# Performance work log

Hardware: AMD Instinct MI355X
Metric: run time of the kernel (lower is better)

The kernel has to match this reference:

```python
import jax, jax.numpy as jnp
import numpy as np

MARGIN = 1.0


def setup_inputs() -> dict:
    key = jax.random.key(0)
    k1, k2 = jax.random.split(key)
    embeddings = jax.random.normal(k1, (4096, 512), dtype=jnp.float32)
    labels = jax.random.randint(k2, (4096,), 0, 256, dtype=jnp.int32)
    return {"embeddings": embeddings, "labels": labels}


def _masked_random_gather(dist, mask, key):
    # Uniformly sample one valid (masked-True) column per row via argmax of
    # uniform noise restricted to the mask (equivalent to torch.randint over
    # the per-row index list, fully vectorized). Rows with no valid entry -> 0.
    B = dist.shape[0]
    u = jax.random.uniform(key, mask.shape)          # [B, B] in [0, 1)
    idx = jnp.argmax(jnp.where(mask, u, -1.0), axis=1)  # [B]
    has_valid = jnp.any(mask, axis=1)
    d = dist[jnp.arange(B), idx]
    return jnp.where(has_valid, d, 0.0)


def reference(embeddings, labels):
    B = embeddings.shape[0]
    # Pairwise squared Euclidean distances: ||a||^2 + ||b||^2 - 2 a.b, clamped >= 0
    dot = embeddings @ embeddings.T                  # [B, B]
    sq = jnp.diagonal(dot)                           # [B]
    dist = jax.nn.relu(sq[None, :] + sq[:, None] - 2.0 * dot)

    same = labels[:, None] == labels[None, :]        # [B, B]
    eye = jnp.eye(B, dtype=bool)
    mask_pos = same & ~eye
    mask_neg = ~same

    kp, kn = jax.random.split(jax.random.key(42))
    positive_dist = _masked_random_gather(dist, mask_pos, kp)
    negative_dist = _masked_random_gather(dist, mask_neg, kn)

    triplet_loss = jax.nn.relu(positive_dist - negative_dist + MARGIN)
    valid = jnp.sum(triplet_loss > 1e-16)
    return jnp.where(valid == 0, jnp.float32(0.0), jnp.mean(triplet_loss))
```

## Files before the change

### kernel.cpp

```cpp
#include <hip/hip_runtime.h>
#include <stdint.h>

#define B 4096
#define D 512

#define NB_NEG 2048

__host__ __device__ __forceinline__ uint32_t rotl32(uint32_t x, int d) {
#ifdef __HIP_DEVICE_COMPILE__
    return __builtin_amdgcn_alignbit(x, x, (uint32_t)(32 - d));
#else
    return (x << d) | (x >> (32 - d));
#endif
}

__host__ __device__ __forceinline__ void tf2x32(uint32_t k0, uint32_t k1,
                                                uint32_t x0, uint32_t x1,
                                                uint32_t& o0, uint32_t& o1) {
    const uint32_t k2 = k0 ^ k1 ^ 0x1BD11BDAu;
#define TF_ROUND(r) { x0 += x1; x1 = rotl32(x1, r); x1 ^= x0; }
    x0 += k0; x1 += k1;
    TF_ROUND(13) TF_ROUND(15) TF_ROUND(26) TF_ROUND(6)
    x0 += k1; x1 += k2 + 1u;
    TF_ROUND(17) TF_ROUND(29) TF_ROUND(16) TF_ROUND(24)
    x0 += k2; x1 += k0 + 2u;
    TF_ROUND(13) TF_ROUND(15) TF_ROUND(26) TF_ROUND(6)
    x0 += k0; x1 += k1 + 3u;
    TF_ROUND(17) TF_ROUND(29) TF_ROUND(16) TF_ROUND(24)
    x0 += k1; x1 += k2 + 4u;
    TF_ROUND(13) TF_ROUND(15) TF_ROUND(26) TF_ROUND(6)
    x0 += k2; x1 += k0 + 5u;
#undef TF_ROUND
    o0 = x0; o1 = x1;
}

__device__ __forceinline__ uint32_t draw32(uint32_t k0, uint32_t k1,
                                           uint32_t flat) {
    uint32_t o0, o1;
    tf2x32(k0, k1, 0u, flat, o0, o1);
    return o0 ^ o1;
}

__device__ __forceinline__ unsigned long long umax64(unsigned long long a,
                                                     unsigned long long b) {
    return a > b ? a : b;
}

__device__ __forceinline__ unsigned long long packbest(int bestv, int bestc) {
    return (bestv < 0)
               ? 0ull
               : ((((unsigned long long)(uint32_t)bestv + 1ull) << 12) |
                  (unsigned long long)(uint32_t)(4095 - bestc));
}

__global__ __launch_bounds__(256) void neg_bucket_kernel(
        const int* __restrict__ labels, int* __restrict__ idxn,
        int* __restrict__ bstart, unsigned short* __restrict__ bcols,
        uint32_t kn0, uint32_t kn1) {
    __shared__ int cnt[256];
    __shared__ int basex[256];
    __shared__ int fillc[256];
    __shared__ unsigned long long red[2][4];

    const int bid = blockIdx.x;
    const int t = threadIdx.x;
    const int lane = t & 63;
    const int w = t >> 6;

    if (bid == 0) {
        const int4* lp = (const int4*)(labels + (t << 4));
        const int4 La = lp[0], Lb = lp[1], Lc = lp[2], Ld = lp[3];
        const int lab16[16] = {La.x, La.y, La.z, La.w, Lb.x, Lb.y, Lb.z, Lb.w,
                               Lc.x, Lc.y, Lc.z, Lc.w, Ld.x, Ld.y, Ld.z, Ld.w};
        cnt[t] = 0;
        fillc[t] = 0;
        __syncthreads();
#pragma unroll
        for (int j = 0; j < 16; ++j) atomicAdd(&cnt[lab16[j]], 1);
        __syncthreads();
        basex[t] = cnt[t];
        __syncthreads();
        for (int off = 1; off < 256; off <<= 1) {
            const int u = (t >= off) ? basex[t - off] : 0;
            __syncthreads();
            basex[t] += u;
            __syncthreads();
        }
        bstart[t] = basex[t] - cnt[t];
        if (t == 255) bstart[256] = B;
#pragma unroll
        for (int j = 0; j < 16; ++j) {
            const int l = lab16[j];
            const int off = atomicAdd(&fillc[l], 1);
            bcols[basex[l] - cnt[l] + off] = (unsigned short)((t << 4) + j);
        }
        __syncthreads();
    }

    const int r0 = bid * 2;
    const int4* lp = (const int4*)(labels + (t << 4));
    const int4 La = lp[0], Lb = lp[1], Lc = lp[2], Ld = lp[3];
    const int lab16[16] = {La.x, La.y, La.z, La.w, Lb.x, Lb.y, Lb.z, Lb.w,
                           Lc.x, Lc.y, Lc.z, Lc.w, Ld.x, Ld.y, Ld.z, Ld.w};
    const int labr0 = labels[r0];
    const int labr1 = labels[r0 + 1];
    const uint32_t f0 = ((uint32_t)r0 << 12) + ((uint32_t)t << 4);
    int bv0 = -1, bc0 = 0, bv1 = -1, bc1 = 0;
#pragma unroll
    for (int j = 0; j < 16; ++j) {
        const int c = (t << 4) + j;
        const uint32_t h0 = draw32(kn0, kn1, f0 + (uint32_t)j);
        const uint32_t h1 = draw32(kn0, kn1, f0 + (uint32_t)j + 4096u);
        const int v0 = (int)(h0 >> 9);
        const int v1 = (int)(h1 >> 9);
        if ((lab16[j] != labr0) & (v0 > bv0)) { bv0 = v0; bc0 = c; }
        if ((lab16[j] != labr1) & (v1 > bv1)) { bv1 = v1; bc1 = c; }
    }
    unsigned long long p0 = packbest(bv0, bc0);
    unsigned long long p1 = packbest(bv1, bc1);
#pragma unroll
    for (int off = 32; off > 0; off >>= 1) {
        p0 = umax64(p0, __shfl_down(p0, off));
        p1 = umax64(p1, __shfl_down(p1, off));
    }
    if (lane == 0) { red[0][w] = p0; red[1][w] = p1; }
    __syncthreads();
    if (t < 2) {
        unsigned long long best = red[t][0];
#pragma unroll
        for (int k = 1; k < 4; ++k) best = umax64(best, red[t][k]);
        idxn[r0 + t] = best ? (int)(4095u - (uint32_t)(best & 0xFFFull)) : -1;
    }
}

__global__ __launch_bounds__(256) void loss_kernel(
        const float* __restrict__ E, const int* __restrict__ labels,
        const int* __restrict__ bstart, const unsigned short* __restrict__ bcols,
        const int* __restrict__ idxn, float* __restrict__ tl,
        uint32_t kp0, uint32_t kp1) {
    const int lane = threadIdx.x & 63;
    const int w = threadIdx.x >> 6;
    const int r = blockIdx.x * 4 + w;

    const int l = labels[r];
    const int s0 = bstart[l];
    const int s1 = bstart[l + 1];
    const uint32_t rbase = (uint32_t)r << 12;
    unsigned long long best = 0ull;
    for (int i = s0 + lane; i < s1; i += 64) {
        const int c = (int)bcols[i];
        if (c == r) continue;
        const uint32_t bits = draw32(kp0, kp1, rbase + (uint32_t)c);
        const unsigned long long pack =
            ((((unsigned long long)(bits >> 9)) + 1ull) << 12) |
            (unsigned long long)(uint32_t)(4095 - c);
        best = umax64(best, pack);
    }
#pragma unroll
    for (int off = 32; off > 0; off >>= 1)
        best = umax64(best, __shfl_xor(best, off));
    const int ip = best ? (int)(4095u - (uint32_t)(best & 0xFFFull)) : -1;
    const int in_ = idxn[r];

    const float4* er = (const float4*)(E + (size_t)r * D);
    float4 a0 = er[lane * 2];
    float4 a1 = er[lane * 2 + 1];
    float aa = a0.x * a0.x + a0.y * a0.y + a0.z * a0.z + a0.w * a0.w +
               a1.x * a1.x + a1.y * a1.y + a1.z * a1.z + a1.w * a1.w;
    float dp = 0.f, pp = 0.f, dn = 0.f, nn = 0.f;
    if (ip >= 0) {
        const float4* ep = (const float4*)(E + (size_t)ip * D);
        float4 b0 = ep[lane * 2];
        float4 b1 = ep[lane * 2 + 1];
        dp = a0.x * b0.x + a0.y * b0.y + a0.z * b0.z + a0.w * b0.w +
             a1.x * b1.x + a1.y * b1.y + a1.z * b1.z + a1.w * b1.w;
        pp = b0.x * b0.x + b0.y * b0.y + b0.z * b0.z + b0.w * b0.w +
             b1.x * b1.x + b1.y * b1.y + b1.z * b1.z + b1.w * b1.w;
    }
    if (in_ >= 0) {
        const float4* en = (const float4*)(E + (size_t)in_ * D);
        float4 c0 = en[lane * 2];
        float4 c1 = en[lane * 2 + 1];
        dn = a0.x * c0.x + a0.y * c0.y + a0.z * c0.z + a0.w * c0.w +
             a1.x * c1.x + a1.y * c1.y + a1.z * c1.z + a1.w * c1.w;
        nn = c0.x * c0.x + c0.y * c0.y + c0.z * c0.z + c0.w * c0.w +
             c1.x * c1.x + c1.y * c1.y + c1.z * c1.z + c1.w * c1.w;
    }
#pragma unroll
    for (int off = 32; off > 0; off >>= 1) {
        aa += __shfl_down(aa, off);
        dp += __shfl_down(dp, off);
        pp += __shfl_down(pp, off);
        dn += __shfl_down(dn, off);
        nn += __shfl_down(nn, off);
    }
    if (lane == 0) {
        const float pd = (ip >= 0) ? fmaxf(aa + pp - 2.0f * dp, 0.f) : 0.f;
        const float nd = (in_ >= 0) ? fmaxf(aa + nn - 2.0f * dn, 0.f) : 0.f;
        tl[r] = fmaxf(pd - nd + 1.0f, 0.f);
    }
}

__global__ __launch_bounds__(256) void finalize_kernel(
        const float* __restrict__ tl, float* __restrict__ out) {
    const int t = threadIdx.x;
    float s = 0.f;
    int c = 0;
    for (int j = t; j < B; j += 256) {
        const float v = tl[j];
        s += v;
        if (v > 1e-16f) c++;
    }
#pragma unroll
    for (int off = 32; off > 0; off >>= 1) {
        s += __shfl_down(s, off);
        c += __shfl_down(c, off);
    }
    __shared__ float ss[4];
    __shared__ int sc[4];
    if ((t & 63) == 0) { ss[t >> 6] = s; sc[t >> 6] = c; }
    __syncthreads();
    if (t == 0) {
#pragma unroll
        for (int k = 1; k < 4; ++k) { s += ss[k]; c += sc[k]; }
        out[0] = (c == 0) ? 0.0f : s * (1.0f / 4096.0f);
    }
}

extern "C" void kernel_launch(void* const* d_in, const int* in_sizes, int n_in,
                              void* d_out, int out_size, void* d_ws,
                              size_t ws_size, hipStream_t stream) {
    const float* E = (const float*)d_in[0];
    const int* labels = (const int*)d_in[1];
    float* out = (float*)d_out;

    char* ws = (char*)d_ws;
    int* idxn = (int*)(ws);
    float* tl = (float*)(ws + 16384);
    int* bstart = (int*)(ws + 32768);
    unsigned short* bcols = (unsigned short*)(ws + 36864);

    uint32_t kp0, kp1, kn0, kn1;
    tf2x32(0u, 42u, 0u, 0u, kp0, kp1);
    tf2x32(0u, 42u, 0u, 1u, kn0, kn1);

    neg_bucket_kernel<<<NB_NEG, 256, 0, stream>>>(labels, idxn, bstart, bcols,
                                                  kn0, kn1);
    loss_kernel<<<B / 4, 256, 0, stream>>>(E, labels, bstart, bcols, idxn, tl,
                                           kp0, kp1);
    finalize_kernel<<<1, 256, 0, stream>>>(tl, out);
}
```

Measured before the change: 47.23 us.

## Fuse negative sampling, positive sampling and loss into one kernel

Merges the negative-sampling kernel and the loss kernel into one kernel that handles two rows per block. The per-label bucket build is dropped; positive sampling now scans the labels each thread already holds and draws random numbers only for same-label columns. Only warps 0-1 of each block then compute the distances. This removes a kernel launch, the bucket-building serial block and the global idx round trip, but leaves two of four warps idle in the distance phase and adds a divergent per-column branch in the positive loop.

```diff
diff --git a/kernel.cpp b/kernel.cpp
--- a/kernel.cpp
+++ b/kernel.cpp
@@ -53,49 +53,18 @@
                   (unsigned long long)(uint32_t)(4095 - bestc));
 }
 
-__global__ __launch_bounds__(256) void neg_bucket_kernel(
-        const int* __restrict__ labels, int* __restrict__ idxn,
-        int* __restrict__ bstart, unsigned short* __restrict__ bcols,
-        uint32_t kn0, uint32_t kn1) {
-    __shared__ int cnt[256];
-    __shared__ int basex[256];
-    __shared__ int fillc[256];
-    __shared__ unsigned long long red[2][4];
+__global__ __launch_bounds__(256) void fused_kernel(
+        const float* __restrict__ E, const int* __restrict__ labels,
+        float* __restrict__ tl, uint32_t kp0, uint32_t kp1, uint32_t kn0,
+        uint32_t kn1) {
+    __shared__ unsigned long long redn[2][4];
+    __shared__ unsigned long long redp[2][4];
+    __shared__ int sidx[4];
 
     const int bid = blockIdx.x;
     const int t = threadIdx.x;
     const int lane = t & 63;
     const int w = t >> 6;
-
-    if (bid == 0) {
-        const int4* lp = (const int4*)(labels + (t << 4));
-        const int4 La = lp[0], Lb = lp[1], Lc = lp[2], Ld = lp[3];
-        const int lab16[16] = {La.x, La.y, La.z, La.w, Lb.x, Lb.y, Lb.z, Lb.w,
-                               Lc.x, Lc.y, Lc.z, Lc.w, Ld.x, Ld.y, Ld.z, Ld.w};
-        cnt[t] = 0;
-        fillc[t] = 0;
-        __syncthreads();
-#pragma unroll
-        for (int j = 0; j < 16; ++j) atomicAdd(&cnt[lab16[j]], 1);
-        __syncthreads();
-        basex[t] = cnt[t];
-        __syncthreads();
-        for (int off = 1; off < 256; off <<= 1) {
-            const int u = (t >= off) ? basex[t - off] : 0;
-            __syncthreads();
-            basex[t] += u;
-            __syncthreads();
-        }
-        bstart[t] = basex[t] - cnt[t];
-        if (t == 255) bstart[256] = B;
-#pragma unroll
-        for (int j = 0; j < 16; ++j) {
-            const int l = lab16[j];
-            const int off = atomicAdd(&fillc[l], 1);
-            bcols[basex[l] - cnt[l] + off] = (unsigned short)((t << 4) + j);
-        }
-        __syncthreads();
-    }
 
     const int r0 = bid * 2;
     const int4* lp = (const int4*)(labels + (t << 4));
@@ -105,6 +74,7 @@
     const int labr0 = labels[r0];
     const int labr1 = labels[r0 + 1];
     const uint32_t f0 = ((uint32_t)r0 << 12) + ((uint32_t)t << 4);
+
     int bv0 = -1, bc0 = 0, bv1 = -1, bc1 = 0;
 #pragma unroll
     for (int j = 0; j < 16; ++j) {
@@ -116,88 +86,95 @@
         if ((lab16[j] != labr0) & (v0 > bv0)) { bv0 = v0; bc0 = c; }
         if ((lab16[j] != labr1) & (v1 > bv1)) { bv1 = v1; bc1 = c; }
     }
-    unsigned long long p0 = packbest(bv0, bc0);
-    unsigned long long p1 = packbest(bv1, bc1);
+
+    int pv0 = -1, pc0 = 0, pv1 = -1, pc1 = 0;
+#pragma unroll 1
+    for (int j = 0; j < 16; ++j) {
+        const int c = (t << 4) + j;
+        const bool m0 = (lab16[j] == labr0) && (c != r0);
+        const bool m1 = (lab16[j] == labr1) && (c != r0 + 1);
+        if (m0) {
+            const uint32_t h = draw32(kp0, kp1, f0 + (uint32_t)j);
+            const int v = (int)(h >> 9);
+            if (v > pv0) { pv0 = v; pc0 = c; }
+        }
+        if (m1) {
+            const uint32_t h = draw32(kp0, kp1, f0 + (uint32_t)j + 4096u);
+            const int v = (int)(h >> 9);
+            if (v > pv1) { pv1 = v; pc1 = c; }
+        }
+    }
+
+    unsigned long long n0 = packbest(bv0, bc0);
+    unsigned long long n1 = packbest(bv1, bc1);
+    unsigned long long q0 = packbest(pv0, pc0);
+    unsigned long long q1 = packbest(pv1, pc1);
 #pragma unroll
     for (int off = 32; off > 0; off >>= 1) {
-        p0 = umax64(p0, __shfl_down(p0, off));
-        p1 = umax64(p1, __shfl_down(p1, off));
-    }
-    if (lane == 0) { red[0][w] = p0; red[1][w] = p1; }
+        n0 = umax64(n0, __shfl_down(n0, off));
+        n1 = umax64(n1, __shfl_down(n1, off));
+        q0 = umax64(q0, __shfl_down(q0, off));
+        q1 = umax64(q1, __shfl_down(q1, off));
+    }
+    if (lane == 0) {
+        redn[0][w] = n0; redn[1][w] = n1;
+        redp[0][w] = q0; redp[1][w] = q1;
+    }
     __syncthreads();
     if (t < 2) {
-        unsigned long long best = red[t][0];
-#pragma unroll
-        for (int k = 1; k < 4; ++k) best = umax64(best, red[t][k]);
-        idxn[r0 + t] = best ? (int)(4095u - (uint32_t)(best & 0xFFFull)) : -1;
-    }
-}
-
-__global__ __launch_bounds__(256) void loss_kernel(
-        const float* __restrict__ E, const int* __restrict__ labels,
-        const int* __restrict__ bstart, const unsigned short* __restrict__ bcols,
-        const int* __restrict__ idxn, float* __restrict__ tl,
-        uint32_t kp0, uint32_t kp1) {
-    const int lane = threadIdx.x & 63;
-    const int w = threadIdx.x >> 6;
-    const int r = blockIdx.x * 4 + w;
-
-    const int l = labels[r];
-    const int s0 = bstart[l];
-    const int s1 = bstart[l + 1];
-    const uint32_t rbase = (uint32_t)r << 12;
-    unsigned long long best = 0ull;
-    for (int i = s0 + lane; i < s1; i += 64) {
-        const int c = (int)bcols[i];
-        if (c == r) continue;
-        const uint32_t bits = draw32(kp0, kp1, rbase + (uint32_t)c);
-        const unsigned long long pack =
-            ((((unsigned long long)(bits >> 9)) + 1ull) << 12) |
-            (unsigned long long)(uint32_t)(4095 - c);
-        best = umax64(best, pack);
-    }
-#pragma unroll
-    for (int off = 32; off > 0; off >>= 1)
-        best = umax64(best, __shfl_xor(best, off));
-    const int ip = best ? (int)(4095u - (uint32_t)(best & 0xFFFull)) : -1;
-    const int in_ = idxn[r];
-
-    const float4* er = (const float4*)(E + (size_t)r * D);
-    float4 a0 = er[lane * 2];
-    float4 a1 = er[lane * 2 + 1];
-    float aa = a0.x * a0.x + a0.y * a0.y + a0.z * a0.z + a0.w * a0.w +
-               a1.x * a1.x + a1.y * a1.y + a1.z * a1.z + a1.w * a1.w;
-    float dp = 0.f, pp = 0.f, dn = 0.f, nn = 0.f;
-    if (ip >= 0) {
-        const float4* ep = (const float4*)(E + (size_t)ip * D);
-        float4 b0 = ep[lane * 2];
-        float4 b1 = ep[lane * 2 + 1];
-        dp = a0.x * b0.x + a0.y * b0.y + a0.z * b0.z + a0.w * b0.w +
-             a1.x * b1.x + a1.y * b1.y + a1.z * b1.z + a1.w * b1.w;
-        pp = b0.x * b0.x + b0.y * b0.y + b0.z * b0.z + b0.w * b0.w +
-             b1.x * b1.x + b1.y * b1.y + b1.z * b1.z + b1.w * b1.w;
-    }
-    if (in_ >= 0) {
-        const float4* en = (const float4*)(E + (size_t)in_ * D);
-        float4 c0 = en[lane * 2];
-        float4 c1 = en[lane * 2 + 1];
-        dn = a0.x * c0.x + a0.y * c0.y + a0.z * c0.z + a0.w * c0.w +
-             a1.x * c1.x + a1.y * c1.y + a1.z * c1.z + a1.w * c1.w;
-        nn = c0.x * c0.x + c0.y * c0.y + c0.z * c0.z + c0.w * c0.w +
-             c1.x * c1.x + c1.y * c1.y + c1.z * c1.z + c1.w * c1.w;
-    }
-#pragma unroll
-    for (int off = 32; off > 0; off >>= 1) {
-        aa += __shfl_down(aa, off);
-        dp += __shfl_down(dp, off);
-        pp += __shfl_down(pp, off);
-        dn += __shfl_down(dn, off);
-        nn += __shfl_down(nn, off);
-    }
-    if (lane == 0) {
-        const float pd = (ip >= 0) ? fmaxf(aa + pp - 2.0f * dp, 0.f) : 0.f;
-        const float nd = (in_ >= 0) ? fmaxf(aa + nn - 2.0f * dn, 0.f) : 0.f;
-        tl[r] = fmaxf(pd - nd + 1.0f, 0.f);
+        unsigned long long bn = redn[t][0];
+        unsigned long long bp = redp[t][0];
+#pragma unroll
+        for (int k = 1; k < 4; ++k) {
+            bn = umax64(bn, redn[t][k]);
+            bp = umax64(bp, redp[t][k]);
+        }
+        sidx[t] = bp ? (int)(4095u - (uint32_t)(bp & 0xFFFull)) : -1;
+        sidx[2 + t] = bn ? (int)(4095u - (uint32_t)(bn & 0xFFFull)) : -1;
+    }
+    __syncthreads();
+
+    if (w < 2) {
+        const int r = r0 + w;
+        const int ip = sidx[w];
+        const int in_ = sidx[2 + w];
+        const float4* er = (const float4*)(E + (size_t)r * D);
+        float4 a0 = er[lane * 2];
+        float4 a1 = er[lane * 2 + 1];
+        float aa = a0.x * a0.x + a0.y * a0.y + a0.z * a0.z + a0.w * a0.w +
+                   a1.x * a1.x + a1.y * a1.y + a1.z * a1.z + a1.w * a1.w;
+        float dp = 0.f, pp = 0.f, dn = 0.f, nn = 0.f;
+        if (ip >= 0) {
+            const float4* ep = (const float4*)(E + (size_t)ip * D);
+            float4 b0 = ep[lane * 2];
+            float4 b1 = ep[lane * 2 + 1];
+            dp = a0.x * b0.x + a0.y * b0.y + a0.z * b0.z + a0.w * b0.w +
+                 a1.x * b1.x + a1.y * b1.y + a1.z * b1.z + a1.w * b1.w;
+            pp = b0.x * b0.x + b0.y * b0.y + b0.z * b0.z + b0.w * b0.w +
+                 b1.x * b1.x + b1.y * b1.y + b1.z * b1.z + b1.w * b1.w;
+        }
+        if (in_ >= 0) {
+            const float4* en = (const float4*)(E + (size_t)in_ * D);
+            float4 c0 = en[lane * 2];
+            float4 c1 = en[lane * 2 + 1];
+            dn = a0.x * c0.x + a0.y * c0.y + a0.z * c0.z + a0.w * c0.w +
+                 a1.x * c1.x + a1.y * c1.y + a1.z * c1.z + a1.w * c1.w;
+            nn = c0.x * c0.x + c0.y * c0.y + c0.z * c0.z + c0.w * c0.w +
+                 c1.x * c1.x + c1.y * c1.y + c1.z * c1.z + c1.w * c1.w;
+        }
+#pragma unroll
+        for (int off = 32; off > 0; off >>= 1) {
+            aa += __shfl_down(aa, off);
+            dp += __shfl_down(dp, off);
+            pp += __shfl_down(pp, off);
+            dn += __shfl_down(dn, off);
+            nn += __shfl_down(nn, off);
+        }
+        if (lane == 0) {
+            const float pd = (ip >= 0) ? fmaxf(aa + pp - 2.0f * dp, 0.f) : 0.f;
+            const float nd = (in_ >= 0) ? fmaxf(aa + nn - 2.0f * dn, 0.f) : 0.f;
+            tl[r] = fmaxf(pd - nd + 1.0f, 0.f);
+        }
     }
 }
 
@@ -234,19 +211,13 @@
     const int* labels = (const int*)d_in[1];
     float* out = (float*)d_out;
 
-    char* ws = (char*)d_ws;
-    int* idxn = (int*)(ws);
-    float* tl = (float*)(ws + 16384);
-    int* bstart = (int*)(ws + 32768);
-    unsigned short* bcols = (unsigned short*)(ws + 36864);
+    float* tl = (float*)d_ws;
 
     uint32_t kp0, kp1, kn0, kn1;
     tf2x32(0u, 42u, 0u, 0u, kp0, kp1);
     tf2x32(0u, 42u, 0u, 1u, kn0, kn1);
 
-    neg_bucket_kernel<<<NB_NEG, 256, 0, stream>>>(labels, idxn, bstart, bcols,
-                                                  kn0, kn1);
-    loss_kernel<<<B / 4, 256, 0, stream>>>(E, labels, bstart, bcols, idxn, tl,
-                                           kp0, kp1);
+    fused_kernel<<<NB_NEG, 256, 0, stream>>>(E, labels, tl, kp0, kp1, kn0,
+                                             kn1);
     finalize_kernel<<<1, 256, 0, stream>>>(tl, out);
 }
```

Measured after the change: 59.10 us. 25.1% more time.
